# Kernel tuning notes

Hardware: AMD Instinct MI355X
Metric: run time of the kernel (lower is better)

Reference implementation:

```python
import jax, jax.numpy as jnp
import numpy as np

EMBED = 1024
HEADS = 16
HEAD_DIM = EMBED // HEADS
B, S = 4, 2048


def setup_inputs() -> dict:
    key = jax.random.key(0)
    ks = jax.random.split(key, 8)
    values = jax.random.normal(ks[0], (B, S, EMBED), dtype=jnp.float32)
    keys_in = jax.random.normal(ks[1], (B, S, EMBED), dtype=jnp.float32)
    query = jax.random.normal(ks[2], (B, S, EMBED), dtype=jnp.float32)
    mask = jnp.ones((B, 1, 1, S), dtype=jnp.int32)
    sc = 1.0 / np.sqrt(HEAD_DIM)
    Wv = jax.random.normal(ks[3], (HEAD_DIM, HEAD_DIM), dtype=jnp.float32) * sc
    Wk = jax.random.normal(ks[4], (HEAD_DIM, HEAD_DIM), dtype=jnp.float32) * sc
    Wq = jax.random.normal(ks[5], (HEAD_DIM, HEAD_DIM), dtype=jnp.float32) * sc
    Wo = jax.random.normal(ks[6], (EMBED, EMBED), dtype=jnp.float32) * (1.0 / np.sqrt(EMBED))
    bo = jnp.zeros((EMBED,), dtype=jnp.float32)
    return {"values": values, "keys": keys_in, "query": query, "mask": mask,
            "Wv": Wv, "Wk": Wk, "Wq": Wq, "Wo": Wo, "bo": bo}


def reference(values, keys, query, mask, Wv, Wk, Wq, Wo, bo):
    n = query.shape[0]
    vl, kl, ql = values.shape[1], keys.shape[1], query.shape[1]
    h, d = HEADS, HEAD_DIM
    # split heads: [n, len, h, d]
    v = values.reshape(n, vl, h, d)
    k = keys.reshape(n, kl, h, d)
    q = query.reshape(n, ql, h, d)
    # per-head linear projections (torch Linear: x @ W.T), shared across heads
    v = jnp.einsum('nlhd,ed->nlhe', v, Wv)
    k = jnp.einsum('nlhd,ed->nlhe', k, Wk)
    q = jnp.einsum('nlhd,ed->nlhe', q, Wq)
    # attention scores [n, h, q, k]
    energy = jnp.einsum('nqhd,nkhd->nhqk', q, k)
    energy = jnp.where(mask == 0, jnp.float32(-1e20), energy)
    # NOTE: original scales by sqrt(embed_size), not sqrt(head_dim)
    attn = jax.nn.softmax(energy / jnp.sqrt(jnp.float32(EMBED)), axis=3)
    out = jnp.einsum('nhql,nlhd->nqhd', attn, v).reshape(n, ql, h * d)
    return out @ Wo.T + bo
```

## Files before the change

### kernel.cpp

```cpp
#include <hip/hip_runtime.h>
#include <hip/hip_bf16.h>


#define SS 2048
#define HH 16
#define DD 64

typedef __attribute__((ext_vector_type(8))) short bf16x8;
typedef __attribute__((ext_vector_type(4))) short s16x4;
typedef __attribute__((ext_vector_type(4))) float f32x4;
typedef __attribute__((ext_vector_type(16))) float f32x16;

#define MFMA32(A, B, C) __builtin_amdgcn_mfma_f32_32x32x16_bf16((A), (B), (C), 0, 0, 0)

__device__ __forceinline__ short f2bf(float f) {
  union { float f; unsigned u; } c; c.f = f;
  unsigned r = (c.u + 0x7FFFu + ((c.u >> 16) & 1u)) >> 16;
  return (short)r;
}

__device__ __forceinline__ int cvtpk(float lo, float hi) {
  int r;
  asm("v_cvt_pk_bf16_f32 %0, %1, %2" : "=v"(r) : "v"(lo), "v"(hi));
  return r;
}

__device__ __forceinline__ float fexp2(float x) {
  float r;
  asm("v_exp_f32 %0, %1" : "=v"(r) : "v"(x));
  return r;
}

__global__ __launch_bounds__(256) void proj_kernel(
    const float* __restrict__ xq, const float* __restrict__ xk, const float* __restrict__ xv,
    const float* __restrict__ Wq, const float* __restrict__ Wk, const float* __restrict__ Wv,
    short* __restrict__ qp, short* __restrict__ kp, short* __restrict__ vp)
{
  __shared__ short xlds[128][72];
  __shared__ short wlds[3][64][72];
  const int t = threadIdx.x;
  const int lane = t & 63;
  const int w = t >> 6;
  const int l15 = lane & 15, l4 = lane >> 4;

  const float* wsrc[3] = {Wq, Wk, Wv};
#pragma unroll
  for (int z = 0; z < 3; ++z) {
#pragma unroll
    for (int i = 0; i < 4; ++i) {
      int fi = (t + i * 256) * 4;
      int row = fi >> 6, col = fi & 63;
      float4 a = *(const float4*)(wsrc[z] + fi);
      s16x4 sv = { f2bf(a.x), f2bf(a.y), f2bf(a.z), f2bf(a.w) };
      *(s16x4*)&wlds[z][row][col] = sv;
    }
  }

  const long r0 = (long)blockIdx.x * 128;
  const float* xin[3] = {xq, xk, xv};
  short* outp[3] = {qp, kp, vp};
  const float SCQ = 0.03125f * 1.4426950408889634f;

#pragma unroll
  for (int z = 0; z < 3; ++z) {
    __syncthreads();
    const float* src = xin[z] + r0 * 64;
#pragma unroll
    for (int i = 0; i < 8; ++i) {
      int fi = (t + i * 256) * 4;
      int row = fi >> 6, col = fi & 63;
      float4 a = *(const float4*)(src + fi);
      s16x4 sv = { f2bf(a.x), f2bf(a.y), f2bf(a.z), f2bf(a.w) };
      *(s16x4*)&xlds[row][col] = sv;
    }
    __syncthreads();

    bf16x8 af[2][2];
#pragma unroll
    for (int mi = 0; mi < 2; ++mi)
#pragma unroll
      for (int kb = 0; kb < 2; ++kb)
        af[mi][kb] = *(const bf16x8*)&xlds[w * 32 + mi * 16 + l15][kb * 32 + l4 * 8];

    f32x4 acc[2][4];
#pragma unroll
    for (int mi = 0; mi < 2; ++mi)
#pragma unroll
      for (int nt = 0; nt < 4; ++nt)
        acc[mi][nt] = (f32x4){0.f, 0.f, 0.f, 0.f};

#pragma unroll
    for (int nt = 0; nt < 4; ++nt)
#pragma unroll
      for (int kb = 0; kb < 2; ++kb) {
        bf16x8 bfr = *(const bf16x8*)&wlds[z][nt * 16 + l15][kb * 32 + l4 * 8];
#pragma unroll
        for (int mi = 0; mi < 2; ++mi)
          acc[mi][nt] = __builtin_amdgcn_mfma_f32_16x16x32_bf16(af[mi][kb], bfr, acc[mi][nt], 0, 0, 0);
      }

    short* dst = outp[z];
    const float sc = (z == 0) ? SCQ : 1.0f;
#pragma unroll
    for (int mi = 0; mi < 2; ++mi)
#pragma unroll
      for (int nt = 0; nt < 4; ++nt)
#pragma unroll
        for (int j = 0; j < 4; ++j) {
          int r = (int)r0 + w * 32 + mi * 16 + l4 * 4 + j;
          int e = nt * 16 + l15;
          int h = r & 15, bs = r >> 4;
          int b = bs >> 11, s = bs & 2047;
          dst[(((long)(b * 16 + h) * 2048 + s) << 6) + e] = f2bf(acc[mi][nt][j] * sc);
        }
  }
}

__global__ __launch_bounds__(256) void wo_cvt(const float* __restrict__ Wo,
                                              short* __restrict__ wob) {
  long i = ((long)blockIdx.x * 256 + threadIdx.x) * 4;
  float4 a = *(const float4*)(Wo + i);
  s16x4 sv = { f2bf(a.x), f2bf(a.y), f2bf(a.z), f2bf(a.w) };
  *(s16x4*)(wob + i) = sv;
}

__global__ __launch_bounds__(256) void vt_kernel(const short* __restrict__ vp,
                                                 short* __restrict__ vpt) {
  __shared__ short tl[64][72];
  const int t = threadIdx.x;
  const long base_in = (long)blockIdx.y * SS * DD + (long)blockIdx.x * 64 * DD;
#pragma unroll
  for (int i = 0; i < 2; ++i) {
    int c = t + i * 256;
    int s = c >> 3, d0 = (c & 7) * 8;
    bf16x8 v = *(const bf16x8*)(vp + base_in + s * 64 + d0);
#pragma unroll
    for (int j = 0; j < 8; ++j) tl[d0 + j][s] = v[j];
  }
  __syncthreads();
  const long base_out = (long)blockIdx.y * DD * SS + (long)blockIdx.x * 64;
#pragma unroll
  for (int i = 0; i < 2; ++i) {
    int c = t + i * 256;
    int d = c >> 3, s0 = (c & 7) * 8;
    *(bf16x8*)(vpt + base_out + (long)d * SS + s0) = *(const bf16x8*)&tl[d][s0];
  }
}

#define SM_CHUNK(SRC, O, A0, A1, A2, A3, PA)                                   \
  do {                                                                         \
    float e0 = fexp2((SRC)[(O) + 0]), e1 = fexp2((SRC)[(O) + 1]);              \
    float e2 = fexp2((SRC)[(O) + 2]), e3 = fexp2((SRC)[(O) + 3]);              \
    float e4 = fexp2((SRC)[(O) + 4]), e5 = fexp2((SRC)[(O) + 5]);              \
    float e6 = fexp2((SRC)[(O) + 6]), e7 = fexp2((SRC)[(O) + 7]);              \
    A0 += e0; A1 += e1; A2 += e2; A3 += e3;                                    \
    A0 += e4; A1 += e5; A2 += e6; A3 += e7;                                    \
    (PA).wd[0] = cvtpk(e0, e1); (PA).wd[1] = cvtpk(e2, e3);                    \
    (PA).wd[2] = cvtpk(e4, e5); (PA).wd[3] = cvtpk(e6, e7);                    \
  } while (0)

__global__ __launch_bounds__(256, 2) void attn_kernel(
    const short* __restrict__ qp, const short* __restrict__ kp, const short* __restrict__ vpt,
    const int* __restrict__ mask, short* __restrict__ ao)
{
  __shared__ short klds[2][64][68];
  __shared__ short vtlds[2][64][68];
  __shared__ int tile_ok[32];
  const int t = threadIdx.x, lane = t & 63, w = t >> 6;
  const int l31 = lane & 31, hi = lane >> 5;
  const int wg = (blockIdx.x & 7) * 64 + (blockIdx.x >> 3);
  const int bh = wg >> 3, qt = wg & 7;
  const int b = bh >> 4, h = bh & 15;
  const short* qb  = qp + (long)bh * SS * DD;
  const short* kbp = kp + (long)bh * SS * DD;
  const short* vtp = vpt + (long)bh * DD * SS;
  const int* mb = mask + b * SS;

  if (t < 32) tile_ok[t] = 1;
  __syncthreads();
  {
    int ok = 1;
#pragma unroll
    for (int i = 0; i < 8; ++i) ok &= (mb[t * 8 + i] != 0);
    if (!ok) tile_ok[t >> 3] = 0;
  }

  const int q0 = qt * 256 + w * 64;
  bf16x8 qf[2][4];
#pragma unroll
  for (int f = 0; f < 2; ++f)
#pragma unroll
    for (int dblk = 0; dblk < 4; ++dblk)
      qf[f][dblk] = *(const bf16x8*)(qb + (long)(q0 + f * 32 + l31) * 64 + dblk * 16 + hi * 8);

  const int sr = t >> 2;
  const int sc = (t & 3) * 16;
  const int v5 = sr & 31;
  const int prow = (sr & 32) + (v5 & 3) + 4 * ((v5 >> 3) & 1)
                 + 8 * (2 * ((v5 >> 4) & 1) + ((v5 >> 2) & 1));
  const short* kr_ptr = kbp + (long)sr * 64 + sc;
  const short* vr_ptr = vtp + (long)sr * SS + sc;

  bf16x8 kr0 = *(const bf16x8*)(kr_ptr);
  bf16x8 kr1 = *(const bf16x8*)(kr_ptr + 8);
  bf16x8 vr0 = *(const bf16x8*)(vr_ptr);
  bf16x8 vr1 = *(const bf16x8*)(vr_ptr + 8);
  *(bf16x8*)&klds[0][prow][sc]      = kr0;
  *(bf16x8*)&klds[0][prow][sc + 8]  = kr1;
  *(bf16x8*)&vtlds[0][sr][sc]       = vr0;
  *(bf16x8*)&vtlds[0][sr][sc + 8]   = vr1;
  kr0 = *(const bf16x8*)(kr_ptr + 4096);
  kr1 = *(const bf16x8*)(kr_ptr + 4096 + 8);
  vr0 = *(const bf16x8*)(vr_ptr + 64);
  vr1 = *(const bf16x8*)(vr_ptr + 64 + 8);

  const f32x16 fzero = {0.f,0.f,0.f,0.f,0.f,0.f,0.f,0.f,
                        0.f,0.f,0.f,0.f,0.f,0.f,0.f,0.f};
  f32x16 oacc[2][2];
#pragma unroll
  for (int f = 0; f < 2; ++f) { oacc[f][0] = fzero; oacc[f][1] = fzero; }
  float l0 = 0.f, l1 = 0.f;

  union PW { int wd[4]; bf16x8 v; };

  for (int kt = 0; kt < SS / 64; ++kt) {
    const int cur = kt & 1, nxt = cur ^ 1;
    const int k0 = kt * 64;
    __syncthreads();
    *(bf16x8*)&klds[nxt][prow][sc]      = kr0;
    *(bf16x8*)&klds[nxt][prow][sc + 8]  = kr1;
    *(bf16x8*)&vtlds[nxt][sr][sc]       = vr0;
    *(bf16x8*)&vtlds[nxt][sr][sc + 8]   = vr1;

    bf16x8 ka[2][4];
#pragma unroll
    for (int kb = 0; kb < 2; ++kb)
#pragma unroll
      for (int dblk = 0; dblk < 4; ++dblk)
        ka[kb][dblk] = *(const bf16x8*)&klds[cur][kb * 32 + l31][dblk * 16 + hi * 8];
    f32x16 sf00, sf01;
    __builtin_amdgcn_s_setprio(1);
    sf00 = MFMA32(ka[0][0], qf[0][0], fzero);
    sf01 = MFMA32(ka[1][0], qf[0][0], fzero);
#pragma unroll
    for (int dblk = 1; dblk < 4; ++dblk) {
      sf00 = MFMA32(ka[0][dblk], qf[0][dblk], sf00);
      sf01 = MFMA32(ka[1][dblk], qf[0][dblk], sf01);
    }
    __builtin_amdgcn_s_setprio(0);

    {
      const int ktn = (kt < 30) ? kt + 2 : 31;
      const long k0n = (long)ktn * 64;
      kr0 = *(const bf16x8*)(kr_ptr + k0n * 64);
      kr1 = *(const bf16x8*)(kr_ptr + k0n * 64 + 8);
      vr0 = *(const bf16x8*)(vr_ptr + k0n);
      vr1 = *(const bf16x8*)(vr_ptr + k0n + 8);
    }

    if (!tile_ok[kt]) {
#pragma unroll
      for (int r = 0; r < 16; ++r) {
        int kvb = k0 + 16 * ((r >> 3) & 1) + 8 * hi + 4 * ((r >> 2) & 1) + (r & 3);
        if (mb[kvb] == 0) sf00[r] = -1e30f;
        if (mb[kvb + 32] == 0) sf01[r] = -1e30f;
      }
    }

    f32x16 sf10, sf11;
    float a0 = 0.f, a1 = 0.f, a2 = 0.f, a3 = 0.f;
    PW pa0[4], pa1[4];
    sf10 = MFMA32(ka[0][0], qf[1][0], fzero);
    sf11 = MFMA32(ka[1][0], qf[1][0], fzero);
    SM_CHUNK(sf00, 0, a0, a1, a2, a3, pa0[0]);
    sf10 = MFMA32(ka[0][1], qf[1][1], sf10);
    sf11 = MFMA32(ka[1][1], qf[1][1], sf11);
    SM_CHUNK(sf00, 8, a0, a1, a2, a3, pa0[1]);
    sf10 = MFMA32(ka[0][2], qf[1][2], sf10);
    sf11 = MFMA32(ka[1][2], qf[1][2], sf11);
    SM_CHUNK(sf01, 0, a0, a1, a2, a3, pa0[2]);
    sf10 = MFMA32(ka[0][3], qf[1][3], sf10);
    sf11 = MFMA32(ka[1][3], qf[1][3], sf11);
    SM_CHUNK(sf01, 8, a0, a1, a2, a3, pa0[3]);
    {
      float sum = (a0 + a1) + (a2 + a3);
      sum += __shfl_xor(sum, 32);
      l0 += sum;
    }

    if (!tile_ok[kt]) {
#pragma unroll
      for (int r = 0; r < 16; ++r) {
        int kvb = k0 + 16 * ((r >> 3) & 1) + 8 * hi + 4 * ((r >> 2) & 1) + (r & 3);
        if (mb[kvb] == 0) sf10[r] = -1e30f;
        if (mb[kvb + 32] == 0) sf11[r] = -1e30f;
      }
    }

    bf16x8 va[2][4];
    float b0 = 0.f, b1 = 0.f, b2 = 0.f, b3 = 0.f;
    va[0][0] = *(const bf16x8*)&vtlds[cur][l31][hi * 8];
    va[1][0] = *(const bf16x8*)&vtlds[cur][32 + l31][hi * 8];
    oacc[0][0] = MFMA32(va[0][0], pa0[0].v, oacc[0][0]);
    oacc[0][1] = MFMA32(va[1][0], pa0[0].v, oacc[0][1]);
    SM_CHUNK(sf10, 0, b0, b1, b2, b3, pa1[0]);
    va[0][1] = *(const bf16x8*)&vtlds[cur][l31][16 + hi * 8];
    va[1][1] = *(const bf16x8*)&vtlds[cur][32 + l31][16 + hi * 8];
    oacc[0][0] = MFMA32(va[0][1], pa0[1].v, oacc[0][0]);
    oacc[0][1] = MFMA32(va[1][1], pa0[1].v, oacc[0][1]);
    SM_CHUNK(sf10, 8, b0, b1, b2, b3, pa1[1]);
    va[0][2] = *(const bf16x8*)&vtlds[cur][l31][32 + hi * 8];
    va[1][2] = *(const bf16x8*)&vtlds[cur][32 + l31][32 + hi * 8];
    oacc[0][0] = MFMA32(va[0][2], pa0[2].v, oacc[0][0]);
    oacc[0][1] = MFMA32(va[1][2], pa0[2].v, oacc[0][1]);
    SM_CHUNK(sf11, 0, b0, b1, b2, b3, pa1[2]);
    va[0][3] = *(const bf16x8*)&vtlds[cur][l31][48 + hi * 8];
    va[1][3] = *(const bf16x8*)&vtlds[cur][32 + l31][48 + hi * 8];
    oacc[0][0] = MFMA32(va[0][3], pa0[3].v, oacc[0][0]);
    oacc[0][1] = MFMA32(va[1][3], pa0[3].v, oacc[0][1]);
    SM_CHUNK(sf11, 8, b0, b1, b2, b3, pa1[3]);
    {
      float sum = (b0 + b1) + (b2 + b3);
      sum += __shfl_xor(sum, 32);
      l1 += sum;
    }

    __builtin_amdgcn_s_setprio(1);
#pragma unroll
    for (int ks = 0; ks < 4; ++ks) {
      oacc[1][0] = MFMA32(va[0][ks], pa1[ks].v, oacc[1][0]);
      oacc[1][1] = MFMA32(va[1][ks], pa1[ks].v, oacc[1][1]);
    }
    __builtin_amdgcn_s_setprio(0);
  }

#pragma unroll
  for (int f = 0; f < 2; ++f) {
    float inv = 1.f / ((f == 0) ? l0 : l1);
    const int q = q0 + f * 32 + l31;
#pragma unroll
    for (int dt = 0; dt < 2; ++dt)
#pragma unroll
      for (int g = 0; g < 4; ++g) {
        s16x4 sv;
#pragma unroll
        for (int j = 0; j < 4; ++j) sv[j] = f2bf(oacc[f][dt][g * 4 + j] * inv);
        int d0 = dt * 32 + g * 8 + hi * 4;
        *(s16x4*)(ao + (long)(b * SS + q) * 1024 + h * 64 + d0) = sv;
      }
  }
}

__global__ __launch_bounds__(256) void out_gemm(
    const short* __restrict__ ao, const short* __restrict__ wob,
    const float* __restrict__ bo, float* __restrict__ out)
{
  __shared__ short alds[2][128][72];
  __shared__ short blds[2][128][72];
  const int t = threadIdx.x, lane = t & 63, w = t >> 6;
  const int l15 = lane & 15, l4 = lane >> 4;
  const int wm = w >> 1, wn = w & 1;
  const long m0 = (long)blockIdx.y * 128;
  const int n0 = blockIdx.x * 128;

  const int srow = t >> 3;
  const int scol = (t & 7) * 8;

  f32x4 acc[4][4];
#pragma unroll
  for (int mi = 0; mi < 4; ++mi)
#pragma unroll
    for (int ni = 0; ni < 4; ++ni) acc[mi][ni] = (f32x4){0.f, 0.f, 0.f, 0.f};

  bf16x8 ar[4], br[4];
#pragma unroll
  for (int i = 0; i < 4; ++i) {
    int row = srow + i * 32;
    ar[i] = *(const bf16x8*)(ao + (m0 + row) * 1024 + scol);
    br[i] = *(const bf16x8*)(wob + (long)(n0 + row) * 1024 + scol);
  }
#pragma unroll
  for (int i = 0; i < 4; ++i) {
    int row = srow + i * 32;
    *(bf16x8*)&alds[0][row][scol] = ar[i];
    *(bf16x8*)&blds[0][row][scol] = br[i];
  }
#pragma unroll
  for (int i = 0; i < 4; ++i) {
    int row = srow + i * 32;
    ar[i] = *(const bf16x8*)(ao + (m0 + row) * 1024 + 64 + scol);
    br[i] = *(const bf16x8*)(wob + (long)(n0 + row) * 1024 + 64 + scol);
  }

  for (int ki = 0; ki < 16; ++ki) {
    const int cur = ki & 1, nxt = cur ^ 1;
    __syncthreads();
#pragma unroll
    for (int i = 0; i < 4; ++i) {
      int row = srow + i * 32;
      *(bf16x8*)&alds[nxt][row][scol] = ar[i];
      *(bf16x8*)&blds[nxt][row][scol] = br[i];
    }
#pragma unroll
    for (int kb = 0; kb < 2; ++kb) {
      bf16x8 af[4], bfr[4];
#pragma unroll
      for (int mi = 0; mi < 4; ++mi)
        af[mi] = *(const bf16x8*)&alds[cur][wm * 64 + mi * 16 + l15][kb * 32 + l4 * 8];
#pragma unroll
      for (int ni = 0; ni < 4; ++ni)
        bfr[ni] = *(const bf16x8*)&blds[cur][wn * 64 + ni * 16 + l15][kb * 32 + l4 * 8];
#pragma unroll
      for (int mi = 0; mi < 4; ++mi)
#pragma unroll
        for (int ni = 0; ni < 4; ++ni)
          acc[mi][ni] = __builtin_amdgcn_mfma_f32_16x16x32_bf16(af[mi], bfr[ni], acc[mi][ni], 0, 0, 0);
    }
    {
      const int kn = ((ki < 14) ? ki + 2 : 15) * 64;
#pragma unroll
      for (int i = 0; i < 4; ++i) {
        int row = srow + i * 32;
        ar[i] = *(const bf16x8*)(ao + (m0 + row) * 1024 + kn + scol);
        br[i] = *(const bf16x8*)(wob + (long)(n0 + row) * 1024 + kn + scol);
      }
    }
  }
#pragma unroll
  for (int ni = 0; ni < 4; ++ni) {
    float bias = bo[n0 + wn * 64 + ni * 16 + l15];
#pragma unroll
    for (int mi = 0; mi < 4; ++mi)
#pragma unroll
      for (int j = 0; j < 4; ++j)
        out[(m0 + wm * 64 + mi * 16 + l4 * 4 + j) * 1024 + n0 + wn * 64 + ni * 16 + l15] =
            acc[mi][ni][j] + bias;
  }
}

extern "C" void kernel_launch(void* const* d_in, const int* in_sizes, int n_in,
                              void* d_out, int out_size, void* d_ws, size_t ws_size,
                              hipStream_t stream) {
  const float* values = (const float*)d_in[0];
  const float* keys   = (const float*)d_in[1];
  const float* query  = (const float*)d_in[2];
  const int*   mask   = (const int*)d_in[3];
  const float* Wv     = (const float*)d_in[4];
  const float* Wk     = (const float*)d_in[5];
  const float* Wq     = (const float*)d_in[6];
  const float* Wo     = (const float*)d_in[7];
  const float* bo     = (const float*)d_in[8];
  float* out = (float*)d_out;

  const long NTOK = 4L * SS * HH * DD;
  short* qp  = (short*)d_ws;
  short* kp  = qp + NTOK;
  short* vp  = kp + NTOK;
  short* aot = vp + NTOK;
  short* wob = aot + NTOK;
  short* vpt = wob + 1024 * 1024;

  hipLaunchKernelGGL(proj_kernel, dim3(1024), dim3(256), 0, stream,
                     query, keys, values, Wq, Wk, Wv, qp, kp, vp);
  hipLaunchKernelGGL(wo_cvt, dim3(1024), dim3(256), 0, stream, Wo, wob);
  hipLaunchKernelGGL(vt_kernel, dim3(32, 64), dim3(256), 0, stream, vp, vpt);
  hipLaunchKernelGGL(attn_kernel, dim3(512), dim3(256), 0, stream,
                     qp, kp, vpt, mask, aot);
  hipLaunchKernelGGL(out_gemm, dim3(8, 64), dim3(256), 0, stream,
                     aot, wob, bo, out);
}
```

Baseline: 137.0 us.

## Split attention KV range across two wave groups and combine partial outputs

Doubles the attention block to 512 threads. Two groups of four waves each process half of the key/value sequence for the same 256 queries, each with its own double-buffered LDS tiles. At the end, group 1 writes its partial accumulators and row sums to shared memory, and group 0 adds them in before normalizing and storing. This is a split-K flash-attention layout meant to raise the number of waves per CU and hide latency. It costs extra LDS, a combine step and higher register pressure under launch bounds (512,4). The combine skips max rescaling, which is valid only because the softmax here never subtracts a running max.

```diff
diff --git a/kernel.cpp b/kernel.cpp
--- a/kernel.cpp
+++ b/kernel.cpp
@@ -159,15 +159,18 @@
     (PA).wd[2] = cvtpk(e4, e5); (PA).wd[3] = cvtpk(e6, e7);                    \
   } while (0)
 
-__global__ __launch_bounds__(256, 2) void attn_kernel(
+#define KL(G, D) smem[0][G][D]
+#define VL(G, D) smem[1][G][D]
+
+__global__ __launch_bounds__(512, 4) void attn_kernel(
     const short* __restrict__ qp, const short* __restrict__ kp, const short* __restrict__ vpt,
     const int* __restrict__ mask, short* __restrict__ ao)
 {
-  __shared__ short klds[2][64][68];
-  __shared__ short vtlds[2][64][68];
+  __shared__ short smem[2][2][2][64][68];
   __shared__ int tile_ok[32];
   const int t = threadIdx.x, lane = t & 63, w = t >> 6;
   const int l31 = lane & 31, hi = lane >> 5;
+  const int g = w >> 2, wq = w & 3;
   const int wg = (blockIdx.x & 7) * 64 + (blockIdx.x >> 3);
   const int bh = wg >> 3, qt = wg & 7;
   const int b = bh >> 4, h = bh & 15;
@@ -181,11 +184,11 @@
   {
     int ok = 1;
 #pragma unroll
-    for (int i = 0; i < 8; ++i) ok &= (mb[t * 8 + i] != 0);
-    if (!ok) tile_ok[t >> 3] = 0;
-  }
-
-  const int q0 = qt * 256 + w * 64;
+    for (int i = 0; i < 4; ++i) ok &= (mb[t * 4 + i] != 0);
+    if (!ok) tile_ok[t >> 4] = 0;
+  }
+
+  const int q0 = qt * 256 + wq * 64;
   bf16x8 qf[2][4];
 #pragma unroll
   for (int f = 0; f < 2; ++f)
@@ -193,22 +196,24 @@
     for (int dblk = 0; dblk < 4; ++dblk)
       qf[f][dblk] = *(const bf16x8*)(qb + (long)(q0 + f * 32 + l31) * 64 + dblk * 16 + hi * 8);
 
-  const int sr = t >> 2;
-  const int sc = (t & 3) * 16;
+  const int tl = t & 255;
+  const int sr = tl >> 2;
+  const int sc = (tl & 3) * 16;
   const int v5 = sr & 31;
   const int prow = (sr & 32) + (v5 & 3) + 4 * ((v5 >> 3) & 1)
                  + 8 * (2 * ((v5 >> 4) & 1) + ((v5 >> 2) & 1));
-  const short* kr_ptr = kbp + (long)sr * 64 + sc;
-  const short* vr_ptr = vtp + (long)sr * SS + sc;
+  const int tb = g * 16;
+  const short* kr_ptr = kbp + (long)tb * 4096 + (long)sr * 64 + sc;
+  const short* vr_ptr = vtp + (long)sr * SS + tb * 64 + sc;
 
   bf16x8 kr0 = *(const bf16x8*)(kr_ptr);
   bf16x8 kr1 = *(const bf16x8*)(kr_ptr + 8);
   bf16x8 vr0 = *(const bf16x8*)(vr_ptr);
   bf16x8 vr1 = *(const bf16x8*)(vr_ptr + 8);
-  *(bf16x8*)&klds[0][prow][sc]      = kr0;
-  *(bf16x8*)&klds[0][prow][sc + 8]  = kr1;
-  *(bf16x8*)&vtlds[0][sr][sc]       = vr0;
-  *(bf16x8*)&vtlds[0][sr][sc + 8]   = vr1;
+  *(bf16x8*)&KL(g, 0)[prow][sc]      = kr0;
+  *(bf16x8*)&KL(g, 0)[prow][sc + 8]  = kr1;
+  *(bf16x8*)&VL(g, 0)[sr][sc]        = vr0;
+  *(bf16x8*)&VL(g, 0)[sr][sc + 8]    = vr1;
   kr0 = *(const bf16x8*)(kr_ptr + 4096);
   kr1 = *(const bf16x8*)(kr_ptr + 4096 + 8);
   vr0 = *(const bf16x8*)(vr_ptr + 64);
@@ -223,21 +228,22 @@
 
   union PW { int wd[4]; bf16x8 v; };
 
-  for (int kt = 0; kt < SS / 64; ++kt) {
-    const int cur = kt & 1, nxt = cur ^ 1;
+  for (int i = 0; i < 16; ++i) {
+    const int cur = i & 1, nxt = cur ^ 1;
+    const int kt = tb + i;
     const int k0 = kt * 64;
     __syncthreads();
-    *(bf16x8*)&klds[nxt][prow][sc]      = kr0;
-    *(bf16x8*)&klds[nxt][prow][sc + 8]  = kr1;
-    *(bf16x8*)&vtlds[nxt][sr][sc]       = vr0;
-    *(bf16x8*)&vtlds[nxt][sr][sc + 8]   = vr1;
+    *(bf16x8*)&KL(g, nxt)[prow][sc]      = kr0;
+    *(bf16x8*)&KL(g, nxt)[prow][sc + 8]  = kr1;
+    *(bf16x8*)&VL(g, nxt)[sr][sc]        = vr0;
+    *(bf16x8*)&VL(g, nxt)[sr][sc + 8]    = vr1;
 
     bf16x8 ka[2][4];
 #pragma unroll
     for (int kb = 0; kb < 2; ++kb)
 #pragma unroll
       for (int dblk = 0; dblk < 4; ++dblk)
-        ka[kb][dblk] = *(const bf16x8*)&klds[cur][kb * 32 + l31][dblk * 16 + hi * 8];
+        ka[kb][dblk] = *(const bf16x8*)&KL(g, cur)[kb * 32 + l31][dblk * 16 + hi * 8];
     f32x16 sf00, sf01;
     __builtin_amdgcn_s_setprio(1);
     sf00 = MFMA32(ka[0][0], qf[0][0], fzero);
@@ -250,12 +256,11 @@
     __builtin_amdgcn_s_setprio(0);
 
     {
-      const int ktn = (kt < 30) ? kt + 2 : 31;
-      const long k0n = (long)ktn * 64;
-      kr0 = *(const bf16x8*)(kr_ptr + k0n * 64);
-      kr1 = *(const bf16x8*)(kr_ptr + k0n * 64 + 8);
-      vr0 = *(const bf16x8*)(vr_ptr + k0n);
-      vr1 = *(const bf16x8*)(vr_ptr + k0n + 8);
+      const int ofn = (i < 14) ? i + 2 : 15;
+      kr0 = *(const bf16x8*)(kr_ptr + (long)ofn * 4096);
+      kr1 = *(const bf16x8*)(kr_ptr + (long)ofn * 4096 + 8);
+      vr0 = *(const bf16x8*)(vr_ptr + ofn * 64);
+      vr1 = *(const bf16x8*)(vr_ptr + ofn * 64 + 8);
     }
 
     if (!tile_ok[kt]) {
@@ -299,23 +304,23 @@
 
     bf16x8 va[2][4];
     float b0 = 0.f, b1 = 0.f, b2 = 0.f, b3 = 0.f;
-    va[0][0] = *(const bf16x8*)&vtlds[cur][l31][hi * 8];
-    va[1][0] = *(const bf16x8*)&vtlds[cur][32 + l31][hi * 8];
+    va[0][0] = *(const bf16x8*)&VL(g, cur)[l31][hi * 8];
+    va[1][0] = *(const bf16x8*)&VL(g, cur)[32 + l31][hi * 8];
     oacc[0][0] = MFMA32(va[0][0], pa0[0].v, oacc[0][0]);
     oacc[0][1] = MFMA32(va[1][0], pa0[0].v, oacc[0][1]);
     SM_CHUNK(sf10, 0, b0, b1, b2, b3, pa1[0]);
-    va[0][1] = *(const bf16x8*)&vtlds[cur][l31][16 + hi * 8];
-    va[1][1] = *(const bf16x8*)&vtlds[cur][32 + l31][16 + hi * 8];
+    va[0][1] = *(const bf16x8*)&VL(g, cur)[l31][16 + hi * 8];
+    va[1][1] = *(const bf16x8*)&VL(g, cur)[32 + l31][16 + hi * 8];
     oacc[0][0] = MFMA32(va[0][1], pa0[1].v, oacc[0][0]);
     oacc[0][1] = MFMA32(va[1][1], pa0[1].v, oacc[0][1]);
     SM_CHUNK(sf10, 8, b0, b1, b2, b3, pa1[1]);
-    va[0][2] = *(const bf16x8*)&vtlds[cur][l31][32 + hi * 8];
-    va[1][2] = *(const bf16x8*)&vtlds[cur][32 + l31][32 + hi * 8];
+    va[0][2] = *(const bf16x8*)&VL(g, cur)[l31][32 + hi * 8];
+    va[1][2] = *(const bf16x8*)&VL(g, cur)[32 + l31][32 + hi * 8];
     oacc[0][0] = MFMA32(va[0][2], pa0[2].v, oacc[0][0]);
     oacc[0][1] = MFMA32(va[1][2], pa0[2].v, oacc[0][1]);
     SM_CHUNK(sf11, 0, b0, b1, b2, b3, pa1[2]);
-    va[0][3] = *(const bf16x8*)&vtlds[cur][l31][48 + hi * 8];
-    va[1][3] = *(const bf16x8*)&vtlds[cur][32 + l31][48 + hi * 8];
+    va[0][3] = *(const bf16x8*)&VL(g, cur)[l31][48 + hi * 8];
+    va[1][3] = *(const bf16x8*)&VL(g, cur)[32 + l31][48 + hi * 8];
     oacc[0][0] = MFMA32(va[0][3], pa0[3].v, oacc[0][0]);
     oacc[0][1] = MFMA32(va[1][3], pa0[3].v, oacc[0][1]);
     SM_CHUNK(sf11, 8, b0, b1, b2, b3, pa1[3]);
@@ -334,20 +339,52 @@
     __builtin_amdgcn_s_setprio(0);
   }
 
-#pragma unroll
-  for (int f = 0; f < 2; ++f) {
-    float inv = 1.f / ((f == 0) ? l0 : l1);
-    const int q = q0 + f * 32 + l31;
-#pragma unroll
-    for (int dt = 0; dt < 2; ++dt)
-#pragma unroll
-      for (int g = 0; g < 4; ++g) {
-        s16x4 sv;
-#pragma unroll
-        for (int j = 0; j < 4; ++j) sv[j] = f2bf(oacc[f][dt][g * 4 + j] * inv);
-        int d0 = dt * 32 + g * 8 + hi * 4;
-        *(s16x4*)(ao + (long)(b * SS + q) * 1024 + h * 64 + d0) = sv;
-      }
+  __syncthreads();
+  float* cmb = (float*)&smem[0][0][0][0][0];
+  const int pbase = wq * 4352 + lane * 68;
+  if (g == 1) {
+#pragma unroll
+    for (int f = 0; f < 2; ++f)
+#pragma unroll
+      for (int dt = 0; dt < 2; ++dt)
+#pragma unroll
+        for (int c = 0; c < 4; ++c) {
+          f32x4 v = { oacc[f][dt][c * 4 + 0], oacc[f][dt][c * 4 + 1],
+                      oacc[f][dt][c * 4 + 2], oacc[f][dt][c * 4 + 3] };
+          *(f32x4*)&cmb[pbase + (f * 2 + dt) * 16 + c * 4] = v;
+        }
+    cmb[pbase + 64] = l0;
+    cmb[pbase + 65] = l1;
+  }
+  __syncthreads();
+  if (g == 0) {
+    l0 += cmb[pbase + 64];
+    l1 += cmb[pbase + 65];
+#pragma unroll
+    for (int f = 0; f < 2; ++f)
+#pragma unroll
+      for (int dt = 0; dt < 2; ++dt)
+#pragma unroll
+        for (int c = 0; c < 4; ++c) {
+          f32x4 v = *(const f32x4*)&cmb[pbase + (f * 2 + dt) * 16 + c * 4];
+#pragma unroll
+          for (int j = 0; j < 4; ++j) oacc[f][dt][c * 4 + j] += v[j];
+        }
+#pragma unroll
+    for (int f = 0; f < 2; ++f) {
+      float inv = 1.f / ((f == 0) ? l0 : l1);
+      const int q = q0 + f * 32 + l31;
+#pragma unroll
+      for (int dt = 0; dt < 2; ++dt)
+#pragma unroll
+        for (int gg = 0; gg < 4; ++gg) {
+          s16x4 sv;
+#pragma unroll
+          for (int j = 0; j < 4; ++j) sv[j] = f2bf(oacc[f][dt][gg * 4 + j] * inv);
+          int d0 = dt * 32 + gg * 8 + hi * 4;
+          *(s16x4*)(ao + (long)(b * SS + q) * 1024 + h * 64 + d0) = sv;
+        }
+    }
   }
 }
 
@@ -464,7 +501,7 @@
                      query, keys, values, Wq, Wk, Wv, qp, kp, vp);
   hipLaunchKernelGGL(wo_cvt, dim3(1024), dim3(256), 0, stream, Wo, wob);
   hipLaunchKernelGGL(vt_kernel, dim3(32, 64), dim3(256), 0, stream, vp, vpt);
-  hipLaunchKernelGGL(attn_kernel, dim3(512), dim3(256), 0, stream,
+  hipLaunchKernelGGL(attn_kernel, dim3(512), dim3(512), 0, stream,
                      qp, kp, vpt, mask, aot);
   hipLaunchKernelGGL(out_gemm, dim3(8, 64), dim3(256), 0, stream,
                      aot, wob, bo, out);
```

Result: slower. 493.1 us (+259.8%).

## Halve attention workgroup to two waves and single-buffer K/V LDS tiles

Applied to the files above, without the earlier changes.

The attention kernel now launches 1024 workgroups of 128 threads, each covering 128 queries instead of 256, so there are twice as many smaller blocks. The K/V LDS tiles drop from double to single buffering, with a second barrier per iteration, and each thread loads four vectors per tile with a one-tile register prefetch instead of two tiles ahead. The intent is more blocks for better CU balance and lower LDS use for higher occupancy. The cost is twice the K/V global traffic per query, an extra sync per tile, and a shorter prefetch distance.

```diff
diff --git a/kernel.cpp b/kernel.cpp
--- a/kernel.cpp
+++ b/kernel.cpp
@@ -159,17 +159,17 @@
     (PA).wd[2] = cvtpk(e4, e5); (PA).wd[3] = cvtpk(e6, e7);                    \
   } while (0)
 
-__global__ __launch_bounds__(256, 2) void attn_kernel(
+__global__ __launch_bounds__(128, 2) void attn_kernel(
     const short* __restrict__ qp, const short* __restrict__ kp, const short* __restrict__ vpt,
     const int* __restrict__ mask, short* __restrict__ ao)
 {
-  __shared__ short klds[2][64][68];
-  __shared__ short vtlds[2][64][68];
+  __shared__ short klds[64][68];
+  __shared__ short vtlds[64][68];
   __shared__ int tile_ok[32];
   const int t = threadIdx.x, lane = t & 63, w = t >> 6;
   const int l31 = lane & 31, hi = lane >> 5;
-  const int wg = (blockIdx.x & 7) * 64 + (blockIdx.x >> 3);
-  const int bh = wg >> 3, qt = wg & 7;
+  const int wg = (blockIdx.x & 7) * 128 + (blockIdx.x >> 3);
+  const int bh = wg >> 4, qt = wg & 15;
   const int b = bh >> 4, h = bh & 15;
   const short* qb  = qp + (long)bh * SS * DD;
   const short* kbp = kp + (long)bh * SS * DD;
@@ -181,11 +181,11 @@
   {
     int ok = 1;
 #pragma unroll
-    for (int i = 0; i < 8; ++i) ok &= (mb[t * 8 + i] != 0);
-    if (!ok) tile_ok[t >> 3] = 0;
-  }
-
-  const int q0 = qt * 256 + w * 64;
+    for (int i = 0; i < 16; ++i) ok &= (mb[t * 16 + i] != 0);
+    if (!ok) tile_ok[t >> 2] = 0;
+  }
+
+  const int q0 = qt * 128 + w * 64;
   bf16x8 qf[2][4];
 #pragma unroll
   for (int f = 0; f < 2; ++f)
@@ -193,26 +193,20 @@
     for (int dblk = 0; dblk < 4; ++dblk)
       qf[f][dblk] = *(const bf16x8*)(qb + (long)(q0 + f * 32 + l31) * 64 + dblk * 16 + hi * 8);
 
-  const int sr = t >> 2;
-  const int sc = (t & 3) * 16;
-  const int v5 = sr & 31;
-  const int prow = (sr & 32) + (v5 & 3) + 4 * ((v5 >> 3) & 1)
+  const int srow = t & 63;
+  const int sc0 = ((t >> 6) & 1) * 32;
+  const int v5 = srow & 31;
+  const int prow = (srow & 32) + (v5 & 3) + 4 * ((v5 >> 3) & 1)
                  + 8 * (2 * ((v5 >> 4) & 1) + ((v5 >> 2) & 1));
-  const short* kr_ptr = kbp + (long)sr * 64 + sc;
-  const short* vr_ptr = vtp + (long)sr * SS + sc;
-
-  bf16x8 kr0 = *(const bf16x8*)(kr_ptr);
-  bf16x8 kr1 = *(const bf16x8*)(kr_ptr + 8);
-  bf16x8 vr0 = *(const bf16x8*)(vr_ptr);
-  bf16x8 vr1 = *(const bf16x8*)(vr_ptr + 8);
-  *(bf16x8*)&klds[0][prow][sc]      = kr0;
-  *(bf16x8*)&klds[0][prow][sc + 8]  = kr1;
-  *(bf16x8*)&vtlds[0][sr][sc]       = vr0;
-  *(bf16x8*)&vtlds[0][sr][sc + 8]   = vr1;
-  kr0 = *(const bf16x8*)(kr_ptr + 4096);
-  kr1 = *(const bf16x8*)(kr_ptr + 4096 + 8);
-  vr0 = *(const bf16x8*)(vr_ptr + 64);
-  vr1 = *(const bf16x8*)(vr_ptr + 64 + 8);
+  const short* kr_ptr = kbp + (long)srow * 64 + sc0;
+  const short* vr_ptr = vtp + (long)srow * SS + sc0;
+
+  bf16x8 kr[4], vr[4];
+#pragma unroll
+  for (int i = 0; i < 4; ++i) {
+    kr[i] = *(const bf16x8*)(kr_ptr + i * 8);
+    vr[i] = *(const bf16x8*)(vr_ptr + i * 8);
+  }
 
   const f32x16 fzero = {0.f,0.f,0.f,0.f,0.f,0.f,0.f,0.f,
                         0.f,0.f,0.f,0.f,0.f,0.f,0.f,0.f};
@@ -224,20 +218,21 @@
   union PW { int wd[4]; bf16x8 v; };
 
   for (int kt = 0; kt < SS / 64; ++kt) {
-    const int cur = kt & 1, nxt = cur ^ 1;
     const int k0 = kt * 64;
     __syncthreads();
-    *(bf16x8*)&klds[nxt][prow][sc]      = kr0;
-    *(bf16x8*)&klds[nxt][prow][sc + 8]  = kr1;
-    *(bf16x8*)&vtlds[nxt][sr][sc]       = vr0;
-    *(bf16x8*)&vtlds[nxt][sr][sc + 8]   = vr1;
+#pragma unroll
+    for (int i = 0; i < 4; ++i) {
+      *(bf16x8*)&klds[prow][sc0 + i * 8]  = kr[i];
+      *(bf16x8*)&vtlds[srow][sc0 + i * 8] = vr[i];
+    }
+    __syncthreads();
 
     bf16x8 ka[2][4];
 #pragma unroll
     for (int kb = 0; kb < 2; ++kb)
 #pragma unroll
       for (int dblk = 0; dblk < 4; ++dblk)
-        ka[kb][dblk] = *(const bf16x8*)&klds[cur][kb * 32 + l31][dblk * 16 + hi * 8];
+        ka[kb][dblk] = *(const bf16x8*)&klds[kb * 32 + l31][dblk * 16 + hi * 8];
     f32x16 sf00, sf01;
     __builtin_amdgcn_s_setprio(1);
     sf00 = MFMA32(ka[0][0], qf[0][0], fzero);
@@ -250,12 +245,12 @@
     __builtin_amdgcn_s_setprio(0);
 
     {
-      const int ktn = (kt < 30) ? kt + 2 : 31;
-      const long k0n = (long)ktn * 64;
-      kr0 = *(const bf16x8*)(kr_ptr + k0n * 64);
-      kr1 = *(const bf16x8*)(kr_ptr + k0n * 64 + 8);
-      vr0 = *(const bf16x8*)(vr_ptr + k0n);
-      vr1 = *(const bf16x8*)(vr_ptr + k0n + 8);
+      const int ktn = (kt < 31) ? kt + 1 : 31;
+#pragma unroll
+      for (int i = 0; i < 4; ++i) {
+        kr[i] = *(const bf16x8*)(kr_ptr + (long)ktn * 4096 + i * 8);
+        vr[i] = *(const bf16x8*)(vr_ptr + (long)ktn * 64 + i * 8);
+      }
     }
 
     if (!tile_ok[kt]) {
@@ -299,23 +294,23 @@
 
     bf16x8 va[2][4];
     float b0 = 0.f, b1 = 0.f, b2 = 0.f, b3 = 0.f;
-    va[0][0] = *(const bf16x8*)&vtlds[cur][l31][hi * 8];
-    va[1][0] = *(const bf16x8*)&vtlds[cur][32 + l31][hi * 8];
+    va[0][0] = *(const bf16x8*)&vtlds[l31][hi * 8];
+    va[1][0] = *(const bf16x8*)&vtlds[32 + l31][hi * 8];
     oacc[0][0] = MFMA32(va[0][0], pa0[0].v, oacc[0][0]);
     oacc[0][1] = MFMA32(va[1][0], pa0[0].v, oacc[0][1]);
     SM_CHUNK(sf10, 0, b0, b1, b2, b3, pa1[0]);
-    va[0][1] = *(const bf16x8*)&vtlds[cur][l31][16 + hi * 8];
-    va[1][1] = *(const bf16x8*)&vtlds[cur][32 + l31][16 + hi * 8];
+    va[0][1] = *(const bf16x8*)&vtlds[l31][16 + hi * 8];
+    va[1][1] = *(const bf16x8*)&vtlds[32 + l31][16 + hi * 8];
     oacc[0][0] = MFMA32(va[0][1], pa0[1].v, oacc[0][0]);
     oacc[0][1] = MFMA32(va[1][1], pa0[1].v, oacc[0][1]);
     SM_CHUNK(sf10, 8, b0, b1, b2, b3, pa1[1]);
-    va[0][2] = *(const bf16x8*)&vtlds[cur][l31][32 + hi * 8];
-    va[1][2] = *(const bf16x8*)&vtlds[cur][32 + l31][32 + hi * 8];
+    va[0][2] = *(const bf16x8*)&vtlds[l31][32 + hi * 8];
+    va[1][2] = *(const bf16x8*)&vtlds[32 + l31][32 + hi * 8];
     oacc[0][0] = MFMA32(va[0][2], pa0[2].v, oacc[0][0]);
     oacc[0][1] = MFMA32(va[1][2], pa0[2].v, oacc[0][1]);
     SM_CHUNK(sf11, 0, b0, b1, b2, b3, pa1[2]);
-    va[0][3] = *(const bf16x8*)&vtlds[cur][l31][48 + hi * 8];
-    va[1][3] = *(const bf16x8*)&vtlds[cur][32 + l31][48 + hi * 8];
+    va[0][3] = *(const bf16x8*)&vtlds[l31][48 + hi * 8];
+    va[1][3] = *(const bf16x8*)&vtlds[32 + l31][48 + hi * 8];
     oacc[0][0] = MFMA32(va[0][3], pa0[3].v, oacc[0][0]);
     oacc[0][1] = MFMA32(va[1][3], pa0[3].v, oacc[0][1]);
     SM_CHUNK(sf11, 8, b0, b1, b2, b3, pa1[3]);
@@ -464,7 +459,7 @@
                      query, keys, values, Wq, Wk, Wv, qp, kp, vp);
   hipLaunchKernelGGL(wo_cvt, dim3(1024), dim3(256), 0, stream, Wo, wob);
   hipLaunchKernelGGL(vt_kernel, dim3(32, 64), dim3(256), 0, stream, vp, vpt);
-  hipLaunchKernelGGL(attn_kernel, dim3(512), dim3(256), 0, stream,
+  hipLaunchKernelGGL(attn_kernel, dim3(1024), dim3(128), 0, stream,
                      qp, kp, vpt, mask, aot);
   hipLaunchKernelGGL(out_gemm, dim3(8, 64), dim3(256), 0, stream,
                      aot, wob, bo, out);
```

New measurement: 144.0 us. 1.05x slower.
